# Kernel optimization log

Hardware: AMD Instinct MI355X
Metric: run time of the kernel (lower is better)

## Reference

```python
import jax, jax.numpy as jnp
import numpy as np
import math

B, S, D = 4, 2048, 1024
H = 16
DH = D // H  # 64
DFF = 4096
EPS = 1e-5


def layernorm(x, g, b):
    mu = jnp.mean(x, axis=-1, keepdims=True)
    var = jnp.var(x, axis=-1, keepdims=True)
    return (x - mu) * jax.lax.rsqrt(var + EPS) * g + b


def setup_inputs() -> dict:
    key = jax.random.key(0)
    ks = jax.random.split(key, 16)
    s = 0.02
    return {
        "src": jax.random.normal(ks[0], (B, S, D), jnp.float32),
        # per-head q/k/v projections stacked: [H, D, DH]
        "Wq": jax.random.normal(ks[1], (H, D, DH), jnp.float32) * s,
        "bq": jnp.zeros((H, DH), jnp.float32),
        "Wk": jax.random.normal(ks[2], (H, D, DH), jnp.float32) * s,
        "bk": jnp.zeros((H, DH), jnp.float32),
        "Wv": jax.random.normal(ks[3], (H, D, DH), jnp.float32) * s,
        "bv": jnp.zeros((H, DH), jnp.float32),
        "Wo": jax.random.normal(ks[4], (D, D), jnp.float32) * s,
        "bo": jnp.zeros((D,), jnp.float32),
        "ln1_g": jnp.ones((D,), jnp.float32),
        "ln1_b": jnp.zeros((D,), jnp.float32),
        "W1": jax.random.normal(ks[5], (D, DFF), jnp.float32) * s,
        "b1": jnp.zeros((DFF,), jnp.float32),
        "W2": jax.random.normal(ks[6], (DFF, D), jnp.float32) * s,
        "b2": jnp.zeros((D,), jnp.float32),
        "ln2_g": jnp.ones((D,), jnp.float32),
        "ln2_b": jnp.zeros((D,), jnp.float32),
    }


def reference(src, Wq, bq, Wk, bk, Wv, bv, Wo, bo, ln1_g, ln1_b,
              W1, b1, W2, b2, ln2_g, ln2_b):
    # Batched equivalent of the per-head Python loop (no causal mask: mask=False)
    q = jnp.einsum('bsd,hde->bhse', src, Wq) + bq[None, :, None, :]
    k = jnp.einsum('bsd,hde->bhse', src, Wk) + bk[None, :, None, :]
    v = jnp.einsum('bsd,hde->bhse', src, Wv) + bv[None, :, None, :]
    scores = jnp.einsum('bhse,bhte->bhst', q, k) / math.sqrt(DH)
    attn = jax.nn.softmax(scores, axis=-1)
    ctx = jnp.einsum('bhst,bhte->bhse', attn, v)  # [B,H,S,DH]
    # cat over heads on last dim == transpose then merge
    ctx = ctx.transpose(0, 2, 1, 3).reshape(B, S, D)
    attn_out = ctx @ Wo + bo
    x1 = layernorm(attn_out + src, ln1_g, ln1_b)
    ffn = jax.nn.relu(x1 @ W1 + b1) @ W2 + b2
    return layernorm(ffn + x1, ln2_g, ln2_b)
```

## Files before the change

### kernel.cpp

```cpp
#include <hip/hip_runtime.h>
#include <stdint.h>

#define DEV __device__ __forceinline__

typedef float f32x4 __attribute__((ext_vector_type(4)));
typedef __bf16 bf16x8 __attribute__((ext_vector_type(8)));
typedef unsigned short u16x4 __attribute__((ext_vector_type(4)));
typedef unsigned short u16x8 __attribute__((ext_vector_type(8)));

DEV unsigned short f2bf(float f) {
  unsigned u = __builtin_bit_cast(unsigned, f);
  u += 0x7fffu + ((u >> 16) & 1u);
  return (unsigned short)(u >> 16);
}
DEV float bf2f(unsigned short h) {
  unsigned u = ((unsigned)h) << 16;
  return __builtin_bit_cast(float, u);
}
DEV void gload_lds16(const void* g, void* l) {
  __builtin_amdgcn_global_load_lds((const __attribute__((address_space(1))) void*)g,
                                   (__attribute__((address_space(3))) void*)l, 16, 0, 0);
}

__global__ void cvt_f32_bf16(const float* __restrict__ in, unsigned short* __restrict__ out, int n) {
  int i = (blockIdx.x * 256 + threadIdx.x) * 4;
  if (i >= n) return;
  f32x4 v = *(const f32x4*)(in + i);
  u16x4 o;
  o[0] = f2bf(v[0]); o[1] = f2bf(v[1]); o[2] = f2bf(v[2]); o[3] = f2bf(v[3]);
  *(u16x4*)(out + i) = o;
}

__global__ void transpose_cvt(const float* __restrict__ src, unsigned short* __restrict__ dst,
                              int R, int C) {
  __shared__ __align__(16) float t[64][65];
  const int tid = threadIdx.x;
  const int r0 = blockIdx.x * 64, c0 = blockIdx.y * 64;
  const int rr = tid >> 2, q = tid & 3;
  const float* s = src + (size_t)(r0 + rr) * C + c0 + q * 16;
#pragma unroll
  for (int j = 0; j < 4; ++j) {
    f32x4 v = *(const f32x4*)(s + j * 4);
    t[rr][q * 16 + j * 4 + 0] = v[0];
    t[rr][q * 16 + j * 4 + 1] = v[1];
    t[rr][q * 16 + j * 4 + 2] = v[2];
    t[rr][q * 16 + j * 4 + 3] = v[3];
  }
  __syncthreads();
  const int cc = tid >> 2, qq = tid & 3;
  unsigned short* o = dst + (size_t)(c0 + cc) * R + r0 + qq * 16;
  u16x8 a, b;
#pragma unroll
  for (int j = 0; j < 8; ++j) {
    a[j] = f2bf(t[qq * 16 + j][cc]);
    b[j] = f2bf(t[qq * 16 + 8 + j][cc]);
  }
  *(u16x8*)o = a;
  *(u16x8*)(o + 8) = b;
}

__global__ void pack_qkv_w(const float* __restrict__ Wq, const float* __restrict__ Wk,
                           const float* __restrict__ Wv, unsigned short* __restrict__ dst) {
  __shared__ __align__(16) float t[64][65];
  const int tid = threadIdx.x;
  const int z = blockIdx.z, part = z >> 4, h = z & 15;
  const float* src = (part == 0 ? Wq : (part == 1 ? Wk : Wv)) + (size_t)h * 65536;
  const int r0 = blockIdx.x * 64;
  const int rr = tid >> 2, q = tid & 3;
  const float* s = src + (size_t)(r0 + rr) * 64 + q * 16;
#pragma unroll
  for (int j = 0; j < 4; ++j) {
    f32x4 v = *(const f32x4*)(s + j * 4);
    t[rr][q * 16 + j * 4 + 0] = v[0];
    t[rr][q * 16 + j * 4 + 1] = v[1];
    t[rr][q * 16 + j * 4 + 2] = v[2];
    t[rr][q * 16 + j * 4 + 3] = v[3];
  }
  __syncthreads();
  const int cc = tid >> 2, qq = tid & 3;
  unsigned short* o = dst + ((size_t)(part * 1024 + h * 64 + cc)) * 1024 + r0 + qq * 16;
  u16x8 a, b;
#pragma unroll
  for (int j = 0; j < 8; ++j) {
    a[j] = f2bf(t[qq * 16 + j][cc]);
    b[j] = f2bf(t[qq * 16 + 8 + j][cc]);
  }
  *(u16x8*)o = a;
  *(u16x8*)(o + 8) = b;
}

__global__ void pack_bias(const float* __restrict__ bq, const float* __restrict__ bk,
                          const float* __restrict__ bv, float* __restrict__ o) {
  int i = blockIdx.x * 256 + threadIdx.x;
  o[i] = i < 1024 ? bq[i] : (i < 2048 ? bk[i - 1024] : bv[i - 2048]);
}

__global__ void vtrans(const unsigned short* __restrict__ v, unsigned short* __restrict__ vt) {
  __shared__ __align__(16) unsigned short t[64][72];
  const int tid = threadIdx.x;
  const int bh = blockIdx.y, s0 = blockIdx.x * 64;
  const int r = tid >> 2, q = (tid & 3) * 16;
  const unsigned short* g = v + ((size_t)bh * 2048 + s0 + r) * 64 + q;
  *(u16x8*)&t[r][q] = *(const u16x8*)g;
  *(u16x8*)&t[r][q + 8] = *(const u16x8*)(g + 8);
  __syncthreads();
  const int d = tid >> 2, qq = (tid & 3) * 16;
  unsigned short* o = vt + ((size_t)bh * 64 + d) * 2048 + s0 + qq;
  u16x8 a, b;
#pragma unroll
  for (int j = 0; j < 8; ++j) {
    a[j] = t[qq + j][d];
    b[j] = t[qq + 8 + j][d];
  }
  *(u16x8*)o = a;
  *(u16x8*)(o + 8) = b;
}

template <int MODE>
__global__ __launch_bounds__(256, 2) void gemm_bt(
    const unsigned short* __restrict__ A, const unsigned short* __restrict__ Bt,
    const float* __restrict__ bias, unsigned short* __restrict__ out,
    unsigned short* __restrict__ qb, unsigned short* __restrict__ kb,
    unsigned short* __restrict__ vb, int M, int N, int K) {
  __shared__ __align__(16) char As[16384];
  __shared__ __align__(16) char Bs[16384];
  const int tid = threadIdx.x;
  const int wave = tid >> 6, lane = tid & 63;
  const int lrow = lane & 15;
  const int kof = (lane >> 4) * 16;
  const int m0 = blockIdx.y * 128, n0 = blockIdx.x * 128;
  const int wm = (wave >> 1) * 64, wn = (wave & 1) * 64;
  const int chunkrow = lane >> 3;
  const int colb0 = (lane & 7) * 16;

  f32x4 acc[4][4] = {};

  for (int k0 = 0; k0 < K; k0 += 64) {
#pragma unroll
    for (int c = 0; c < 4; ++c) {
      const int chunk = wave * 4 + c;
      const int rowA = chunk * 8 + chunkrow;
      const int srcb = colb0 ^ ((rowA & 7) << 4);
      const char* ga = (const char*)A + ((size_t)(m0 + rowA) * K + k0) * 2 + srcb;
      const char* gb = (const char*)Bt + ((size_t)(n0 + rowA) * K + k0) * 2 + srcb;
      gload_lds16(ga, As + chunk * 1024);
      gload_lds16(gb, Bs + chunk * 1024);
    }
    __syncthreads();
#pragma unroll
    for (int kk = 0; kk < 2; ++kk) {
      bf16x8 af[4], bv4[4];
#pragma unroll
      for (int i = 0; i < 4; ++i) {
        const int ra = wm + i * 16 + lrow;
        af[i] = *(const bf16x8*)(As + ra * 128 + ((kk * 64 + kof) ^ ((ra & 7) << 4)));
        const int rb = wn + i * 16 + lrow;
        bv4[i] = *(const bf16x8*)(Bs + rb * 128 + ((kk * 64 + kof) ^ ((rb & 7) << 4)));
      }
#pragma unroll
      for (int mi = 0; mi < 4; ++mi)
#pragma unroll
        for (int ni = 0; ni < 4; ++ni)
          acc[mi][ni] = __builtin_amdgcn_mfma_f32_16x16x32_bf16(af[mi], bv4[ni], acc[mi][ni], 0, 0, 0);
    }
    __syncthreads();
  }

#pragma unroll
  for (int mi = 0; mi < 4; ++mi) {
    const int row = m0 + wm + mi * 16 + ((lane >> 4) << 2);
#pragma unroll
    for (int ni = 0; ni < 4; ++ni) {
      const int col = n0 + wn + ni * 16 + lrow;
      const float bvv = bias[col];
#pragma unroll
      for (int r = 0; r < 4; ++r) {
        float v = acc[mi][ni][r] + bvv;
        if (MODE == 1) v = fmaxf(v, 0.0f);
        const int rr = row + r;
        if constexpr (MODE == 2) {
          const int part = col >> 10, cc = col & 1023, h = cc >> 6, e = cc & 63;
          if (part == 0) v *= 0.18033688011112042f;
          unsigned short* dst = part == 0 ? qb : (part == 1 ? kb : vb);
          dst[(((size_t)((rr >> 11) * 16 + h)) * 2048 + (rr & 2047)) * 64 + e] = f2bf(v);
        } else {
          out[(size_t)rr * N + col] = f2bf(v);
        }
      }
    }
  }
}

__global__ __launch_bounds__(256, 3) void attn_kernel(
    const unsigned short* __restrict__ q_buf, const unsigned short* __restrict__ k_buf,
    const unsigned short* __restrict__ vt_buf, unsigned short* __restrict__ ctx) {
  __shared__ __align__(16) char Ks[2][8192];
  __shared__ __align__(16) char Vs[2][8192];
  __shared__ __align__(16) __bf16 Ps[4][32][72];
  const int tid = threadIdx.x, wave = tid >> 6, lane = tid & 63;
  const int wg = (blockIdx.x & 7) * 128 + (blockIdx.x >> 3);
  const int bh = wg >> 4;
  const int q0 = (wg & 15) * 128;
  const int lrow = lane & 15, lg = lane >> 4;

  bf16x8 qf[2][2];
#pragma unroll
  for (int mt = 0; mt < 2; ++mt)
#pragma unroll
    for (int kk = 0; kk < 2; ++kk)
      qf[mt][kk] = *(const bf16x8*)(q_buf +
          ((size_t)bh * 2048 + q0 + wave * 32 + mt * 16 + lrow) * 64 + kk * 32 + lg * 8);

  f32x4 acc_o[2][4] = {};
  f32x4 accd[2] = {};
  bf16x8 ones;
#pragma unroll
  for (int j = 0; j < 8; ++j) ones[j] = (lrow == 0) ? (__bf16)1.0f : (__bf16)0.0f;

  auto stage = [&](int t, int buf) {
#pragma unroll
    for (int i = 0; i < 2; ++i) {
      const int c = i * 256 + wave * 64 + lane;
      const int row = c >> 3;
      const int col = ((c & 7) * 16) ^ ((row & 7) << 4);
      gload_lds16((const char*)k_buf + ((size_t)(bh * 2048 + t * 64 + row)) * 128 + col,
                  &Ks[buf][(i * 256 + wave * 64) * 16]);
      gload_lds16((const char*)vt_buf + ((size_t)(bh * 64 + row)) * 4096 + t * 128 + col,
                  &Vs[buf][(i * 256 + wave * 64) * 16]);
    }
  };

  stage(0, 0);
  for (int t = 0; t < 32; ++t) {
    const int cur = t & 1;
    __syncthreads();
    stage(t < 31 ? t + 1 : 31, cur ^ 1);

    f32x4 sacc[2][4] = {};
#pragma unroll
    for (int kk = 0; kk < 2; ++kk) {
      bf16x8 bfr[4];
#pragma unroll
      for (int nt = 0; nt < 4; ++nt) {
        const int row = nt * 16 + lrow;
        bfr[nt] = *(const bf16x8*)&Ks[cur][row * 128 + ((kk * 64 + lg * 16) ^ ((row & 7) << 4))];
      }
      __builtin_amdgcn_s_setprio(1);
#pragma unroll
      for (int mt = 0; mt < 2; ++mt)
#pragma unroll
        for (int nt = 0; nt < 4; ++nt)
          sacc[mt][nt] = __builtin_amdgcn_mfma_f32_16x16x32_bf16(qf[mt][kk], bfr[nt], sacc[mt][nt], 0, 0, 0);
      __builtin_amdgcn_s_setprio(0);
    }

#pragma unroll
    for (int mt = 0; mt < 2; ++mt)
#pragma unroll
      for (int r = 0; r < 4; ++r) {
        const int ql = mt * 16 + lg * 4 + r;
#pragma unroll
        for (int nt = 0; nt < 4; ++nt)
          Ps[wave][ql][nt * 16 + lrow] = (__bf16)exp2f(sacc[mt][nt][r]);
      }

#pragma unroll
    for (int kk = 0; kk < 2; ++kk) {
      bf16x8 pfr[2], vfr[4];
#pragma unroll
      for (int mt = 0; mt < 2; ++mt)
        pfr[mt] = *(const bf16x8*)&Ps[wave][mt * 16 + lrow][kk * 32 + lg * 8];
#pragma unroll
      for (int nd = 0; nd < 4; ++nd) {
        const int row = nd * 16 + lrow;
        vfr[nd] = *(const bf16x8*)&Vs[cur][row * 128 + ((kk * 64 + lg * 16) ^ ((row & 7) << 4))];
      }
      __builtin_amdgcn_s_setprio(1);
#pragma unroll
      for (int mt = 0; mt < 2; ++mt) {
        accd[mt] = __builtin_amdgcn_mfma_f32_16x16x32_bf16(pfr[mt], ones, accd[mt], 0, 0, 0);
#pragma unroll
        for (int nd = 0; nd < 4; ++nd)
          acc_o[mt][nd] = __builtin_amdgcn_mfma_f32_16x16x32_bf16(pfr[mt], vfr[nd], acc_o[mt][nd], 0, 0, 0);
      }
      __builtin_amdgcn_s_setprio(0);
    }
  }

  const int b = bh >> 4, h = bh & 15;
#pragma unroll
  for (int mt = 0; mt < 2; ++mt)
#pragma unroll
    for (int r = 0; r < 4; ++r) {
      const float den = __shfl(accd[mt][r], lane & 48);
      const float inv = 1.0f / den;
      const int s = q0 + wave * 32 + mt * 16 + lg * 4 + r;
#pragma unroll
      for (int nd = 0; nd < 4; ++nd)
        ctx[((size_t)(b * 2048 + s)) * 1024 + h * 64 + nd * 16 + lrow] =
            f2bf(acc_o[mt][nd][r] * inv);
    }
}

template <bool RES_BF, bool OUT_F32>
__global__ __launch_bounds__(256) void ln_kernel(
    const unsigned short* __restrict__ xin, const void* __restrict__ res,
    const float* __restrict__ g, const float* __restrict__ b, void* __restrict__ out) {
  const int row = blockIdx.x, tid = threadIdx.x;
  const size_t base = (size_t)row * 1024 + tid * 4;
  float x[4];
  u16x4 xv = *(const u16x4*)(xin + base);
  if constexpr (RES_BF) {
    u16x4 rv = *(const u16x4*)((const unsigned short*)res + base);
#pragma unroll
    for (int j = 0; j < 4; ++j) x[j] = bf2f(xv[j]) + bf2f(rv[j]);
  } else {
    f32x4 rv = *(const f32x4*)((const float*)res + base);
#pragma unroll
    for (int j = 0; j < 4; ++j) x[j] = bf2f(xv[j]) + rv[j];
  }
  float s1 = 0.f, s2 = 0.f;
#pragma unroll
  for (int j = 0; j < 4; ++j) { s1 += x[j]; s2 += x[j] * x[j]; }
#pragma unroll
  for (int off = 32; off > 0; off >>= 1) {
    s1 += __shfl_down(s1, off);
    s2 += __shfl_down(s2, off);
  }
  __shared__ float red[8];
  const int wv = tid >> 6, ln = tid & 63;
  if (ln == 0) { red[wv] = s1; red[4 + wv] = s2; }
  __syncthreads();
  s1 = red[0] + red[1] + red[2] + red[3];
  s2 = red[4] + red[5] + red[6] + red[7];
  const float mu = s1 * (1.0f / 1024.0f);
  const float rs = rsqrtf(s2 * (1.0f / 1024.0f) - mu * mu + 1e-5f);
#pragma unroll
  for (int j = 0; j < 4; ++j) {
    const float y = (x[j] - mu) * rs * g[tid * 4 + j] + b[tid * 4 + j];
    if constexpr (OUT_F32) ((float*)out)[base + j] = y;
    else ((unsigned short*)out)[base + j] = f2bf(y);
  }
}

static const size_t OFF_SBF  = 0;
static const size_t OFF_Q    = 16777216;
static const size_t OFF_K    = 33554432;
static const size_t OFF_V    = 50331648;
static const size_t OFF_VT   = 67108864;
static const size_t OFF_WQKV = 83886080;
static const size_t OFF_BQKV = 90177536;
static const size_t OFF_WO   = 90189824;
static const size_t OFF_W1   = 92286976;
static const size_t OFF_W2   = 100675584;
static const size_t OFF_CTX  = 109064192;
static const size_t OFF_AO   = 125841408;
static const size_t OFF_X1   = 142618624;
static const size_t OFF_FFN  = 159395840;

extern "C" void kernel_launch(void* const* d_in, const int* in_sizes, int n_in,
                              void* d_out, int out_size, void* d_ws, size_t ws_size,
                              hipStream_t stream) {
  const float* src = (const float*)d_in[0];
  const float* Wq  = (const float*)d_in[1];
  const float* bq  = (const float*)d_in[2];
  const float* Wk  = (const float*)d_in[3];
  const float* bk  = (const float*)d_in[4];
  const float* Wv  = (const float*)d_in[5];
  const float* bv  = (const float*)d_in[6];
  const float* Wo  = (const float*)d_in[7];
  const float* bo  = (const float*)d_in[8];
  const float* g1  = (const float*)d_in[9];
  const float* be1 = (const float*)d_in[10];
  const float* W1  = (const float*)d_in[11];
  const float* b1  = (const float*)d_in[12];
  const float* W2  = (const float*)d_in[13];
  const float* b2  = (const float*)d_in[14];
  const float* g2  = (const float*)d_in[15];
  const float* be2 = (const float*)d_in[16];

  char* ws = (char*)d_ws;
  unsigned short* sbf  = (unsigned short*)(ws + OFF_SBF);
  unsigned short* h1   = (unsigned short*)(ws + OFF_SBF);
  unsigned short* qb   = (unsigned short*)(ws + OFF_Q);
  unsigned short* kb   = (unsigned short*)(ws + OFF_K);
  unsigned short* vb   = (unsigned short*)(ws + OFF_V);
  unsigned short* vtb  = (unsigned short*)(ws + OFF_VT);
  unsigned short* wqkv = (unsigned short*)(ws + OFF_WQKV);
  float*          bqkv = (float*)(ws + OFF_BQKV);
  unsigned short* wot  = (unsigned short*)(ws + OFF_WO);
  unsigned short* w1t  = (unsigned short*)(ws + OFF_W1);
  unsigned short* w2t  = (unsigned short*)(ws + OFF_W2);
  unsigned short* ctx  = (unsigned short*)(ws + OFF_CTX);
  unsigned short* ao   = (unsigned short*)(ws + OFF_AO);
  unsigned short* x1   = (unsigned short*)(ws + OFF_X1);
  unsigned short* ffn  = (unsigned short*)(ws + OFF_FFN);
  float* outp = (float*)d_out;

  cvt_f32_bf16<<<dim3(8192), dim3(256), 0, stream>>>(src, sbf, 8388608);
  pack_qkv_w<<<dim3(16, 1, 48), dim3(256), 0, stream>>>(Wq, Wk, Wv, wqkv);
  pack_bias<<<dim3(12), dim3(256), 0, stream>>>(bq, bk, bv, bqkv);
  transpose_cvt<<<dim3(16, 16), dim3(256), 0, stream>>>(Wo, wot, 1024, 1024);
  transpose_cvt<<<dim3(16, 64), dim3(256), 0, stream>>>(W1, w1t, 1024, 4096);
  transpose_cvt<<<dim3(64, 16), dim3(256), 0, stream>>>(W2, w2t, 4096, 1024);

  gemm_bt<2><<<dim3(24, 64), dim3(256), 0, stream>>>(sbf, wqkv, bqkv, nullptr, qb, kb, vb,
                                                     8192, 3072, 1024);
  vtrans<<<dim3(32, 64), dim3(256), 0, stream>>>(vb, vtb);
  attn_kernel<<<dim3(1024), dim3(256), 0, stream>>>(qb, kb, vtb, ctx);
  gemm_bt<0><<<dim3(8, 64), dim3(256), 0, stream>>>(ctx, wot, bo, ao, nullptr, nullptr, nullptr,
                                                    8192, 1024, 1024);
  ln_kernel<false, false><<<dim3(8192), dim3(256), 0, stream>>>(ao, src, g1, be1, x1);
  gemm_bt<1><<<dim3(32, 64), dim3(256), 0, stream>>>(x1, w1t, b1, h1, nullptr, nullptr, nullptr,
                                                     8192, 4096, 1024);
  gemm_bt<0><<<dim3(8, 64), dim3(256), 0, stream>>>(h1, w2t, b2, ffn, nullptr, nullptr, nullptr,
                                                    8192, 1024, 4096);
  ln_kernel<true, true><<<dim3(8192), dim3(256), 0, stream>>>(ffn, x1, g2, be2, outp);

  (void)in_sizes; (void)n_in; (void)out_size; (void)ws_size;
}
```

Measured before the change: 398.9 us.

## Compute attention transposed with 32x32 MFMA and keep probabilities in registers

Rewrites the attention inner loop to compute S^T = K·Q^T with 32x32x16 bf16 MFMAs, so the exponentiated scores land in a register layout that can be packed directly as the B operand of the P·V MFMA. This removes the per-wave LDS round trip for P and the extra MFMA against a ones vector that computed the row sums, which are now done with VALU adds plus a cross-half shuffle. Launch bounds are raised to 4 blocks per CU to allow more occupancy. The V fragment reads are now split into two 8-byte LDS loads and assembled in registers.

```diff
diff --git a/kernel.cpp b/kernel.cpp
--- a/kernel.cpp
+++ b/kernel.cpp
@@ -4,9 +4,12 @@
 #define DEV __device__ __forceinline__
 
 typedef float f32x4 __attribute__((ext_vector_type(4)));
+typedef float f32x16 __attribute__((ext_vector_type(16)));
 typedef __bf16 bf16x8 __attribute__((ext_vector_type(8)));
+typedef __bf16 bf16x4 __attribute__((ext_vector_type(4)));
 typedef unsigned short u16x4 __attribute__((ext_vector_type(4)));
 typedef unsigned short u16x8 __attribute__((ext_vector_type(8)));
+typedef unsigned u32x4 __attribute__((ext_vector_type(4)));
 
 DEV unsigned short f2bf(float f) {
   unsigned u = __builtin_bit_cast(unsigned, f);
@@ -16,6 +19,11 @@
 DEV float bf2f(unsigned short h) {
   unsigned u = ((unsigned)h) << 16;
   return __builtin_bit_cast(float, u);
+}
+DEV unsigned pkbf(float lo, float hi) {
+  unsigned r;
+  asm("v_cvt_pk_bf16_f32 %0, %1, %2" : "=v"(r) : "v"(lo), "v"(hi));
+  return r;
 }
 DEV void gload_lds16(const void* g, void* l) {
   __builtin_amdgcn_global_load_lds((const __attribute__((address_space(1))) void*)g,
@@ -191,31 +199,28 @@
   }
 }
 
-__global__ __launch_bounds__(256, 3) void attn_kernel(
+__global__ __launch_bounds__(256, 4) void attn_kernel(
     const unsigned short* __restrict__ q_buf, const unsigned short* __restrict__ k_buf,
     const unsigned short* __restrict__ vt_buf, unsigned short* __restrict__ ctx) {
   __shared__ __align__(16) char Ks[2][8192];
   __shared__ __align__(16) char Vs[2][8192];
-  __shared__ __align__(16) __bf16 Ps[4][32][72];
   const int tid = threadIdx.x, wave = tid >> 6, lane = tid & 63;
   const int wg = (blockIdx.x & 7) * 128 + (blockIdx.x >> 3);
   const int bh = wg >> 4;
   const int q0 = (wg & 15) * 128;
-  const int lrow = lane & 15, lg = lane >> 4;
-
-  bf16x8 qf[2][2];
-#pragma unroll
-  for (int mt = 0; mt < 2; ++mt)
-#pragma unroll
-    for (int kk = 0; kk < 2; ++kk)
-      qf[mt][kk] = *(const bf16x8*)(q_buf +
-          ((size_t)bh * 2048 + q0 + wave * 32 + mt * 16 + lrow) * 64 + kk * 32 + lg * 8);
-
-  f32x4 acc_o[2][4] = {};
-  f32x4 accd[2] = {};
-  bf16x8 ones;
-#pragma unroll
-  for (int j = 0; j < 8; ++j) ones[j] = (lrow == 0) ? (__bf16)1.0f : (__bf16)0.0f;
+  const int l31 = lane & 31, hi = lane >> 5;
+
+  bf16x8 qf[4];
+#pragma unroll
+  for (int kk = 0; kk < 4; ++kk)
+    qf[kk] = *(const bf16x8*)(q_buf +
+        ((size_t)bh * 2048 + q0 + wave * 32 + l31) * 64 + kk * 16 + hi * 8);
+
+  f32x16 acc_o[2] = {};
+  float l_reg = 0.f;
+
+  const int stg_r = tid >> 2;
+  const int stg_p = (tid & 3) * 16;
 
   auto stage = [&](int t, int buf) {
 #pragma unroll
@@ -236,69 +241,81 @@
     __syncthreads();
     stage(t < 31 ? t + 1 : 31, cur ^ 1);
 
-    f32x4 sacc[2][4] = {};
-#pragma unroll
-    for (int kk = 0; kk < 2; ++kk) {
-      bf16x8 bfr[4];
-#pragma unroll
-      for (int nt = 0; nt < 4; ++nt) {
-        const int row = nt * 16 + lrow;
-        bfr[nt] = *(const bf16x8*)&Ks[cur][row * 128 + ((kk * 64 + lg * 16) ^ ((row & 7) << 4))];
+    f32x16 sacc[2] = {};
+#pragma unroll
+    for (int kk = 0; kk < 4; ++kk) {
+      bf16x8 kf[2];
+#pragma unroll
+      for (int mt = 0; mt < 2; ++mt) {
+        const int row = mt * 32 + l31;
+        kf[mt] = *(const bf16x8*)&Ks[cur][row * 128 + ((kk * 32 + hi * 16) ^ ((row & 7) << 4))];
       }
       __builtin_amdgcn_s_setprio(1);
 #pragma unroll
       for (int mt = 0; mt < 2; ++mt)
-#pragma unroll
-        for (int nt = 0; nt < 4; ++nt)
-          sacc[mt][nt] = __builtin_amdgcn_mfma_f32_16x16x32_bf16(qf[mt][kk], bfr[nt], sacc[mt][nt], 0, 0, 0);
+        sacc[mt] = __builtin_amdgcn_mfma_f32_32x32x16_bf16(kf[mt], qf[kk], sacc[mt], 0, 0, 0);
       __builtin_amdgcn_s_setprio(0);
     }
 
 #pragma unroll
     for (int mt = 0; mt < 2; ++mt)
 #pragma unroll
+      for (int r = 0; r < 16; ++r)
+        sacc[mt][r] = exp2f(sacc[mt][r]);
+    {
+      f32x4 s0 = {sacc[0][0], sacc[0][1], sacc[0][2], sacc[0][3]};
+      f32x4 s1 = {sacc[0][4], sacc[0][5], sacc[0][6], sacc[0][7]};
+      f32x4 s2 = {sacc[0][8], sacc[0][9], sacc[0][10], sacc[0][11]};
+      f32x4 s3 = {sacc[0][12], sacc[0][13], sacc[0][14], sacc[0][15]};
+#pragma unroll
       for (int r = 0; r < 4; ++r) {
-        const int ql = mt * 16 + lg * 4 + r;
-#pragma unroll
-        for (int nt = 0; nt < 4; ++nt)
-          Ps[wave][ql][nt * 16 + lrow] = (__bf16)exp2f(sacc[mt][nt][r]);
+        s0[r] += sacc[1][r];  s1[r] += sacc[1][4 + r];
+        s2[r] += sacc[1][8 + r];  s3[r] += sacc[1][12 + r];
       }
-
-#pragma unroll
-    for (int kk = 0; kk < 2; ++kk) {
-      bf16x8 pfr[2], vfr[4];
-#pragma unroll
-      for (int mt = 0; mt < 2; ++mt)
-        pfr[mt] = *(const bf16x8*)&Ps[wave][mt * 16 + lrow][kk * 32 + lg * 8];
-#pragma unroll
-      for (int nd = 0; nd < 4; ++nd) {
-        const int row = nd * 16 + lrow;
-        vfr[nd] = *(const bf16x8*)&Vs[cur][row * 128 + ((kk * 64 + lg * 16) ^ ((row & 7) << 4))];
+      f32x4 s01 = s0 + s1, s23 = s2 + s3;
+      f32x4 sa = s01 + s23;
+      l_reg += (sa[0] + sa[1]) + (sa[2] + sa[3]);
+    }
+
+#pragma unroll
+    for (int g = 0; g < 4; ++g) {
+      const int m = g >> 1, c = g & 1;
+      unsigned w0 = pkbf(sacc[m][8 * c + 0], sacc[m][8 * c + 1]);
+      unsigned w1 = pkbf(sacc[m][8 * c + 2], sacc[m][8 * c + 3]);
+      unsigned w2 = pkbf(sacc[m][8 * c + 4], sacc[m][8 * c + 5]);
+      unsigned w3 = pkbf(sacc[m][8 * c + 6], sacc[m][8 * c + 7]);
+      u32x4 bw = {w0, w1, w2, w3};
+      bf16x8 pb = __builtin_bit_cast(bf16x8, bw);
+      bf16x8 vf[2];
+#pragma unroll
+      for (int mtd = 0; mtd < 2; ++mtd) {
+        const int row = mtd * 32 + l31;
+        const int cb = g * 32 + hi * 8;
+        const int sw = (row & 7) << 4;
+        bf16x4 lo = *(const bf16x4*)&Vs[cur][row * 128 + (cb ^ sw)];
+        bf16x4 hi4 = *(const bf16x4*)&Vs[cur][row * 128 + ((cb + 16) ^ sw)];
+        vf[mtd] = __builtin_shufflevector(lo, hi4, 0, 1, 2, 3, 4, 5, 6, 7);
       }
       __builtin_amdgcn_s_setprio(1);
 #pragma unroll
-      for (int mt = 0; mt < 2; ++mt) {
-        accd[mt] = __builtin_amdgcn_mfma_f32_16x16x32_bf16(pfr[mt], ones, accd[mt], 0, 0, 0);
-#pragma unroll
-        for (int nd = 0; nd < 4; ++nd)
-          acc_o[mt][nd] = __builtin_amdgcn_mfma_f32_16x16x32_bf16(pfr[mt], vfr[nd], acc_o[mt][nd], 0, 0, 0);
-      }
+      for (int mtd = 0; mtd < 2; ++mtd)
+        acc_o[mtd] = __builtin_amdgcn_mfma_f32_32x32x16_bf16(vf[mtd], pb, acc_o[mtd], 0, 0, 0);
       __builtin_amdgcn_s_setprio(0);
     }
   }
 
+  const float den = l_reg + __shfl_xor(l_reg, 32);
+  const float inv = 1.0f / den;
   const int b = bh >> 4, h = bh & 15;
-#pragma unroll
-  for (int mt = 0; mt < 2; ++mt)
-#pragma unroll
-    for (int r = 0; r < 4; ++r) {
-      const float den = __shfl(accd[mt][r], lane & 48);
-      const float inv = 1.0f / den;
-      const int s = q0 + wave * 32 + mt * 16 + lg * 4 + r;
-#pragma unroll
-      for (int nd = 0; nd < 4; ++nd)
-        ctx[((size_t)(b * 2048 + s)) * 1024 + h * 64 + nd * 16 + lrow] =
-            f2bf(acc_o[mt][nd][r] * inv);
+  const size_t orow = ((size_t)(b * 2048 + q0 + wave * 32 + l31)) * 1024 + h * 64;
+#pragma unroll
+  for (int mtd = 0; mtd < 2; ++mtd)
+#pragma unroll
+    for (int gq = 0; gq < 4; ++gq) {
+      u16x4 o;
+#pragma unroll
+      for (int e = 0; e < 4; ++e) o[e] = f2bf(acc_o[mtd][gq * 4 + e] * inv);
+      *(u16x4*)(ctx + orow + mtd * 32 + gq * 8 + hi * 4) = o;
     }
 }
 
```

New measurement: 389.2 us. -2.4%, faster.
